# Optimization experiments

Hardware: AMD Instinct MI355X
Metric: run time of the kernel (lower is better)

The kernel has to match this reference:

```python
import jax, jax.numpy as jnp
import numpy as np

B, S, H, W = 64, 32, 40, 64
SENS, UNITS, MOTOR, NA = 1283, 48, 4, 2
UNFOLDS = 6  # ncps LTC default ode_unfolds
EPS = 1e-8


def setup_inputs() -> dict:
    key = jax.random.key(0)
    ks = iter(jax.random.split(key, 40))
    u = lambda sh, lo, hi: jax.random.uniform(next(ks), sh, jnp.float32, lo, hi)
    inp = {}
    inp["depth_image"] = jax.random.uniform(next(ks), (B, S, H, W), jnp.float32)
    inp["relative_position"] = jax.random.normal(next(ks), (B, S, 3), jnp.float32)
    # CNN params (conv k3 s2 p1 + ReLU) x3: 1->32->64->32
    def cw(o, i):
        return jax.random.normal(next(ks), (o, i, 3, 3), jnp.float32) / np.sqrt(i * 9.0)
    inp["w1"], inp["b1"] = cw(32, 1), jnp.zeros((32,), jnp.float32)
    inp["w2"], inp["b2"] = cw(64, 32), jnp.zeros((64,), jnp.float32)
    inp["w3"], inp["b3"] = cw(32, 64), jnp.zeros((32,), jnp.float32)
    # LTC cell params (ncps init ranges)
    inp["input_w"] = jnp.ones((SENS,), jnp.float32)
    inp["input_b"] = jnp.zeros((SENS,), jnp.float32)
    inp["sens_w"] = u((SENS, UNITS), 0.001, 1.0)
    inp["sens_mu"] = u((SENS, UNITS), 0.3, 0.8)
    inp["sens_sigma"] = u((SENS, UNITS), 3.0, 8.0)
    inp["sens_erev"] = jnp.sign(jax.random.normal(next(ks), (SENS, UNITS)))
    inp["rec_w"] = u((UNITS, UNITS), 0.001, 1.0)
    inp["rec_mu"] = u((UNITS, UNITS), 0.3, 0.8)
    inp["rec_sigma"] = u((UNITS, UNITS), 3.0, 8.0)
    inp["rec_erev"] = jnp.sign(jax.random.normal(next(ks), (UNITS, UNITS)))
    inp["gleak"] = u((UNITS,), 0.001, 1.0)
    inp["vleak"] = u((UNITS,), -0.2, 0.2)
    inp["cm"] = u((UNITS,), 0.4, 0.6)
    inp["out_w"] = jnp.ones((MOTOR,), jnp.float32)
    inp["out_b"] = jnp.zeros((MOTOR,), jnp.float32)
    inp["head_w"] = jax.random.normal(next(ks), (MOTOR, NA), jnp.float32) * 0.5
    inp["head_b"] = jnp.zeros((NA,), jnp.float32)
    inp["sens_mask"] = (jax.random.uniform(next(ks), (SENS, UNITS)) < 0.3).astype(jnp.int32)
    inp["rec_mask"] = (jax.random.uniform(next(ks), (UNITS, UNITS)) < 0.3).astype(jnp.int32)
    return inp


def _conv(x, w, b):
    y = jax.lax.conv_general_dilated(x, w, (2, 2), [(1, 1), (1, 1)],
                                     dimension_numbers=("NCHW", "OIHW", "NCHW"))
    return jax.nn.relu(y + b[None, :, None, None])


def reference(depth_image, relative_position, w1, b1, w2, b2, w3, b3,
              input_w, input_b, sens_w, sens_mu, sens_sigma, sens_erev,
              rec_w, rec_mu, rec_sigma, rec_erev, gleak, vleak, cm,
              out_w, out_b, head_w, head_b, sens_mask, rec_mask):
    b, s = depth_image.shape[:2]
    x = depth_image.reshape(b * s, 1, H, W)
    x = _conv(_conv(_conv(x, w1, b1), w2, b2), w3, b3)  # [b*s,32,5,8]
    feat = x.reshape(b, s, -1)  # [b,s,1280]
    seq = jnp.concatenate([feat, relative_position.reshape(b, s, -1)], axis=2)  # [b,s,1283]

    sp = jax.nn.softplus
    smask = sens_mask.astype(seq.dtype)
    rmask = rec_mask.astype(seq.dtype)
    cm_t = sp(cm) * UNFOLDS          # cm / (elapsed_time / ode_unfolds), dt=1
    gl = sp(gleak)
    sw_pos = sp(sens_w) * smask
    rw_pos = sp(rec_w) * rmask

    def step(v, xt):  # xt: [b, SENS]
        I = xt * input_w + input_b
        # sensory synapse activations: [b, SENS, UNITS]
        sa = sw_pos * jax.nn.sigmoid(sens_sigma * (I[:, :, None] - sens_mu))
        w_num_s = (sa * sens_erev).sum(1)  # [b, UNITS]
        w_den_s = sa.sum(1)
        def unfold(v, _):
            ra = rw_pos * jax.nn.sigmoid(rec_sigma * (v[:, :, None] - rec_mu))
            num = cm_t * v + gl * vleak + (ra * rec_erev).sum(1) + w_num_s
            den = cm_t + gl + ra.sum(1) + w_den_s
            return num / (den + EPS), None
        v, _ = jax.lax.scan(unfold, v, None, length=UNFOLDS)
        y = v[:, :MOTOR] * out_w + out_b  # motor neuron readout
        return v, y

    v0 = jnp.zeros((b, UNITS), seq.dtype)
    _, ys = jax.lax.scan(step, v0, jnp.swapaxes(seq, 0, 1))  # [s, b, MOTOR]
    pooled = ys.mean(0)  # mean over seq dim
    return jnp.tanh(pooled @ head_w + head_b)  # [b, NA] action mean
```

## Files before the change

kernel.cpp:

```cpp
#include <hip/hip_runtime.h>
#include <hip/hip_bf16.h>


typedef __attribute__((ext_vector_type(8))) short bshort8;
typedef __attribute__((ext_vector_type(4))) float f32x4;

constexpr long OFF_SEQ  = 0;
constexpr long OFF_SP4  = 2627584;
constexpr long OFF_RP4  = 2873920;
constexpr long OFF_CM   = 2886208;
constexpr long OFF_W2B  = 2886400;
constexpr long OFF_W3B  = 2898688;
constexpr long OFF_PART = 2907904;

__device__ __forceinline__ float sp_(float x) {
    return fmaxf(x, 0.f) + log1pf(expf(-fabsf(x)));
}

__global__ void prep_kernel(const float* __restrict__ sens_w, const float* __restrict__ sens_mu,
                            const float* __restrict__ sens_sigma, const float* __restrict__ sens_erev,
                            const int* __restrict__ sens_mask,
                            const float* __restrict__ rec_w, const float* __restrict__ rec_mu,
                            const float* __restrict__ rec_sigma, const float* __restrict__ rec_erev,
                            const int* __restrict__ rec_mask,
                            const float* __restrict__ gleak, const float* __restrict__ vleak,
                            const float* __restrict__ cm,
                            const float* __restrict__ w2, const float* __restrict__ w3,
                            float* __restrict__ ws) {
    const float L2E = 1.4426950408889634f;
    int i = blockIdx.x * 256 + threadIdx.x;
    if (i < 61584) {
        float m  = sens_mask[i] ? 1.f : 0.f;
        float sw = sp_(sens_w[i]) * m;
        float sg = sens_sigma[i], mu = sens_mu[i];
        ((float4*)(ws + OFF_SP4))[i] =
            make_float4(-sg * L2E, sg * mu * L2E, sw * sens_erev[i], sw);
    } else if (i < 64656) {
        int q = i - 61584;
        int j = q >> 6, u = q & 63;
        float4 v = make_float4(0.f, 0.f, 0.f, 0.f);
        if (u < 48) {
            int idx = j * 48 + u;
            float m  = rec_mask[idx] ? 1.f : 0.f;
            float sw = sp_(rec_w[idx]) * m;
            float sg = rec_sigma[idx], mu = rec_mu[idx];
            v = make_float4(-sg * L2E, sg * mu * L2E, sw * rec_erev[idx], sw);
        }
        ((float4*)(ws + OFF_RP4))[q] = v;
    } else if (i < 64704) {
        int u = i - 64656;
        float g = sp_(gleak[u]);
        ws[OFF_CM + u]       = sp_(cm[u]) * 6.f;
        ws[OFF_CM + 64 + u]  = g;
        ws[OFF_CM + 128 + u] = g * vleak[u];
    } else if (i < 89280) {
        int n = i - 64704;
        int j = n & 7, l = (n >> 3) & 63, t2 = n >> 9;
        int wv = t2 & 3;
        int r  = t2 >> 2;
        int xp = r & 1, hk = r >> 1;
        int ky = hk % 3, h = hk / 3;
        int oc = wv * 16 + (l & 15);
        int kgB = l >> 4;
        int icl = (kgB & 1) * 8 + j;
        int ic = h * 16 + icl;
        int kx = 2 * xp + (kgB >> 1);
        float val = (kx == 3) ? 0.f : w2[((oc * 32 + ic) * 3 + ky) * 3 + kx];
        ((__hip_bfloat16*)(ws + OFF_W2B))[n] = __float2bfloat16(val);
    } else if (i < 107712) {
        int n = i - 89280;
        int j = n & 7, l = (n >> 3) & 63, t3 = n >> 9;
        int h = t3 & 1, u2 = t3 >> 1;
        int nt = u2 / 9, p = u2 % 9;
        int ky = p / 3, kx = p % 3;
        int oc = nt * 16 + (l & 15);
        int ic = h * 32 + (l >> 4) * 8 + j;
        ((__hip_bfloat16*)(ws + OFF_W3B))[n] =
            __float2bfloat16(w3[((oc * 64 + ic) * 3 + ky) * 3 + kx]);
    }
}

#define IMGB 0
#define C1H  5424
#define A2E  0
#define A2O  12672
#define SMB  28272

__global__ __launch_bounds__(256, 4) void cnn_kernel(
    const float* __restrict__ depth, const float* __restrict__ relpos,
    const float* __restrict__ w1, const float* __restrict__ b1,
    const float* __restrict__ b2, const float* __restrict__ b3,
    const __hip_bfloat16* __restrict__ w2b, const __hip_bfloat16* __restrict__ w3b,
    float* __restrict__ seq) {
    __shared__ __align__(16) char smraw[SMB];
    const int t = threadIdx.x;
    const int img = blockIdx.x;
    const int l = t & 63;
    const int wvu = __builtin_amdgcn_readfirstlane(t >> 6);
    const int m = l & 15, kg = l >> 4;

    for (int i = t; i < 7068; i += 256) ((uint*)smraw)[i] = 0u;
    __syncthreads();
    for (int i = t; i < 1280; i += 256) {
        int pos = 2 * i;
        int h = pos >> 6, w = pos & 63;
        float2 d = *(const float2*)(depth + (long)img * 2560 + pos);
        __hip_bfloat162 pk = __float22bfloat162_rn(d);
        *(__hip_bfloat162*)(smraw + IMGB + ((h + 1) * 66 + (w + 2)) * 2) = pk;
    }
    __syncthreads();

    const __hip_bfloat16* imgp = (const __hip_bfloat16*)(smraw + IMGB);
    f32x4 acc[10];
    {
        float bias = b2[wvu * 16 + m];
#pragma unroll
        for (int mt = 0; mt < 10; ++mt) acc[mt] = (f32x4){bias, bias, bias, bias};
    }

#pragma unroll 1
    for (int h = 0; h < 2; ++h) {
        const int ocb = h * 16 + wvu * 4;
        float wv4[4][9], bv4[4];
#pragma unroll
        for (int j = 0; j < 4; ++j) {
            bv4[j] = b1[ocb + j];
#pragma unroll
            for (int k = 0; k < 9; ++k) wv4[j][k] = w1[(ocb + j) * 9 + k];
        }
#pragma unroll 1
        for (int i = 0; i < 10; ++i) {
            int p = l + (i << 6);
            int y1 = p >> 5, x1 = p & 31;
            float xin[9];
#pragma unroll
            for (int ky = 0; ky < 3; ++ky)
#pragma unroll
                for (int kx = 0; kx < 3; ++kx)
                    xin[ky * 3 + kx] = __bfloat162float(imgp[(2 * y1 + ky) * 66 + 2 * x1 + kx + 1]);
            float o[4];
#pragma unroll
            for (int j = 0; j < 4; ++j) {
                float a = bv4[j];
#pragma unroll
                for (int k = 0; k < 9; ++k) a = fmaf(wv4[j][k], xin[k], a);
                o[j] = fmaxf(a, 0.f);
            }
            char* cb = smraw + C1H + (((y1 + 1) * 34) + (x1 + 1)) * 32 + wvu * 8;
            *(__hip_bfloat162*)cb       = __float22bfloat162_rn(make_float2(o[0], o[1]));
            *(__hip_bfloat162*)(cb + 4) = __float22bfloat162_rn(make_float2(o[2], o[3]));
        }
        bshort8 Bh[6];
#pragma unroll
        for (int f = 0; f < 6; ++f)
            Bh[f] = *(const bshort8*)(w2b + (((h * 6 + f) * 4 + wvu) * 64 + l) * 8);
        __syncthreads();
#pragma unroll
        for (int ky = 0; ky < 3; ++ky) {
#pragma unroll
            for (int xp = 0; xp < 2; ++xp) {
                bshort8 Bp = Bh[ky * 2 + xp];
                const char* base = smraw + C1H + (ky * 34 + 2 * m + 2 * xp + (kg >> 1)) * 32 + (kg & 1) * 16;
#pragma unroll
                for (int mt = 0; mt < 10; ++mt) {
                    bshort8 A = *(const bshort8*)(base + mt * 2176);
                    acc[mt] = __builtin_amdgcn_mfma_f32_16x16x32_bf16(A, Bp, acc[mt], 0, 0, 0);
                }
            }
        }
        __syncthreads();
    }

    for (int i = t; i < 6336; i += 256) ((uint*)smraw)[i] = 0u;
    __syncthreads();
    {
        int oc = wvu * 16 + m;
        int q = oc >> 3, sub = oc & 7;
#pragma unroll
        for (int mt = 0; mt < 10; ++mt) {
            int row = mt + 1;
#pragma unroll
            for (int reg = 0; reg < 4; ++reg) {
                int x2 = kg * 4 + reg;
                int odd = x2 & 1;
                int xi = odd ? ((x2 + 1) >> 1) : (x2 >> 1);
                char* ab = smraw + (odd ? A2O : A2E);
                float v = fmaxf(acc[mt][reg], 0.f);
                *(__hip_bfloat16*)(ab + (((q * 11 + row) * 9 + xi) * 8 + sub) * 2) = __float2bfloat16(v);
            }
        }
    }
    __syncthreads();

    {
        const int nt = wvu & 1;
        const bool two = wvu < 2;
        f32x4 c3a = (f32x4){0.f, 0.f, 0.f, 0.f};
        f32x4 c3b = (f32x4){0.f, 0.f, 0.f, 0.f};
        const int xb = m & 7, yb = m >> 3;
#pragma unroll
        for (int p = 0; p < 9; ++p) {
            int ky = p / 3, kx = p % 3;
            const char* arr = smraw + ((kx == 1) ? A2E : A2O);
            int xi3 = xb + (kx == 2);
#pragma unroll
            for (int h = 0; h < 2; ++h) {
                bshort8 B = *(const bshort8*)(w3b + (((nt * 9 + p) * 2 + h) * 64 + l) * 8);
                int q = h * 4 + kg;
                const char* base = arr + ((q * 11 + 2 * yb + ky) * 9 + xi3) * 16;
                if (two) {
                    bshort8 A0 = *(const bshort8*)(base);
                    c3a = __builtin_amdgcn_mfma_f32_16x16x32_bf16(A0, B, c3a, 0, 0, 0);
                    bshort8 A2 = *(const bshort8*)(base + 1152);
                    c3b = __builtin_amdgcn_mfma_f32_16x16x32_bf16(A2, B, c3b, 0, 0, 0);
                } else {
                    bshort8 A1 = *(const bshort8*)(base + 576);
                    c3a = __builtin_amdgcn_mfma_f32_16x16x32_bf16(A1, B, c3a, 0, 0, 0);
                }
            }
        }
        __syncthreads();
        float* sb = (float*)smraw;
        int oc = nt * 16 + m;
        float bv = b3[oc];
        int ob40 = oc * 40;
        if (two) {
#pragma unroll
            for (int reg = 0; reg < 4; ++reg) {
                sb[ob40 + kg * 4 + reg] = fmaxf(c3a[reg] + bv, 0.f);
                int px2 = 32 + kg * 4 + reg;
                if (px2 < 40) sb[ob40 + px2] = fmaxf(c3b[reg] + bv, 0.f);
            }
        } else {
#pragma unroll
            for (int reg = 0; reg < 4; ++reg)
                sb[ob40 + 16 + kg * 4 + reg] = fmaxf(c3a[reg] + bv, 0.f);
        }
        __syncthreads();
        for (int i = t; i < 1283; i += 256)
            seq[(long)img * 1283 + i] = (i < 1280) ? sb[i] : relpos[img * 3 + (i - 1280)];
    }
}

__global__ __launch_bounds__(768) void sensory_kernel(
    const float* __restrict__ sp, const float* __restrict__ seq,
    const float* __restrict__ iw, const float* __restrict__ ibias,
    float2* __restrict__ part) {
    const float4* P4 = (const float4*)sp;
    __shared__ __align__(16) char sbuf[49152];
    float*  IT  = (float*)sbuf;
    float2* red = (float2*)sbuf;
    const int t = threadIdx.x;
    const int pb = blockIdx.x * 8;

    for (int p = 0; p < 8; ++p)
        for (int k = t; k < 1283; k += 768)
            IT[k * 8 + p] = fmaf(seq[(long)(pb + p) * 1283 + k], iw[k], ibias[k]);
    __syncthreads();

    const int u = t % 48, kg = t / 48;
    float2 acc[8];
#pragma unroll
    for (int p = 0; p < 8; ++p) acc[p] = make_float2(0.f, 0.f);

#pragma unroll 2
    for (int i = 0; i < 81; ++i) {
        int k = kg + 16 * i;
        if (k < 1283) {
            float4 pv = P4[k * 48 + u];
            float4 Ia = *(const float4*)&IT[k * 8];
            float4 Ib = *(const float4*)&IT[k * 8 + 4];
            float r0 = __builtin_amdgcn_rcpf(1.f + __builtin_amdgcn_exp2f(fmaf(pv.x, Ia.x, pv.y)));
            float r1 = __builtin_amdgcn_rcpf(1.f + __builtin_amdgcn_exp2f(fmaf(pv.x, Ia.y, pv.y)));
            float r2 = __builtin_amdgcn_rcpf(1.f + __builtin_amdgcn_exp2f(fmaf(pv.x, Ia.z, pv.y)));
            float r3 = __builtin_amdgcn_rcpf(1.f + __builtin_amdgcn_exp2f(fmaf(pv.x, Ia.w, pv.y)));
            float r4 = __builtin_amdgcn_rcpf(1.f + __builtin_amdgcn_exp2f(fmaf(pv.x, Ib.x, pv.y)));
            float r5 = __builtin_amdgcn_rcpf(1.f + __builtin_amdgcn_exp2f(fmaf(pv.x, Ib.y, pv.y)));
            float r6 = __builtin_amdgcn_rcpf(1.f + __builtin_amdgcn_exp2f(fmaf(pv.x, Ib.z, pv.y)));
            float r7 = __builtin_amdgcn_rcpf(1.f + __builtin_amdgcn_exp2f(fmaf(pv.x, Ib.w, pv.y)));
            acc[0].x = fmaf(pv.z, r0, acc[0].x); acc[0].y = fmaf(pv.w, r0, acc[0].y);
            acc[1].x = fmaf(pv.z, r1, acc[1].x); acc[1].y = fmaf(pv.w, r1, acc[1].y);
            acc[2].x = fmaf(pv.z, r2, acc[2].x); acc[2].y = fmaf(pv.w, r2, acc[2].y);
            acc[3].x = fmaf(pv.z, r3, acc[3].x); acc[3].y = fmaf(pv.w, r3, acc[3].y);
            acc[4].x = fmaf(pv.z, r4, acc[4].x); acc[4].y = fmaf(pv.w, r4, acc[4].y);
            acc[5].x = fmaf(pv.z, r5, acc[5].x); acc[5].y = fmaf(pv.w, r5, acc[5].y);
            acc[6].x = fmaf(pv.z, r6, acc[6].x); acc[6].y = fmaf(pv.w, r6, acc[6].y);
            acc[7].x = fmaf(pv.z, r7, acc[7].x); acc[7].y = fmaf(pv.w, r7, acc[7].y);
        }
    }
    __syncthreads();
#pragma unroll
    for (int p = 0; p < 8; ++p) red[(kg * 8 + p) * 48 + u] = acc[p];
    __syncthreads();
    if (t < 384) {
        int p = t / 48, uu = t - p * 48;
        float sn = 0.f, sd = 0.f;
#pragma unroll
        for (int g = 0; g < 16; ++g) {
            float2 rr = red[(g * 8 + p) * 48 + uu];
            sn += rr.x; sd += rr.y;
        }
        part[(long)(pb + p) * 48 + uu] = make_float2(sn, sd);
    }
}

__global__ __launch_bounds__(512) void recurrent_kernel(
    const float* __restrict__ rp, const float* __restrict__ cmglv,
    const float2* __restrict__ part,
    const float* __restrict__ out_w, const float* __restrict__ out_b,
    const float* __restrict__ head_w, const float* __restrict__ head_b,
    float* __restrict__ outp) {
    const float4* RP4 = (const float4*)rp;
    __shared__ float2 WL[32 * 48];
    __shared__ float2 red[2][8][64];
    __shared__ float ym[4];
    const int t = threadIdx.x, b = blockIdx.x;
    const int u = t & 63;
    const int jg = __builtin_amdgcn_readfirstlane(t >> 6);
    const int j0 = jg * 6;
    const bool uval = u < 48;
    float4 rpj[6];
#pragma unroll
    for (int jj = 0; jj < 6; ++jj) rpj[jj] = RP4[(j0 + jj) * 64 + u];
    for (int i = t; i < 1536; i += 512) WL[i] = part[(long)b * 1536 + i];
    float cmt = 0.f, gl = 0.f, glv = 0.f;
    if (uval) { cmt = cmglv[u]; gl = cmglv[64 + u]; glv = cmglv[128 + u]; }
    float ow = 0.f, ob = 0.f;
    if (jg == 0 && u < 4) { ow = out_w[u]; ob = out_b[u]; }
    __syncthreads();

    float vn = 0.f;
    float yacc = 0.f;
    int buf = 0;
    for (int s = 0; s < 32; ++s) {
        float2 wnd = uval ? WL[s * 48 + u] : make_float2(0.f, 0.f);
#pragma unroll 1
        for (int unf = 0; unf < 6; ++unf) {
            float pn = 0.f, pd = 0.f;
#pragma unroll
            for (int jj = 0; jj < 6; ++jj) {
                float vj = __shfl(vn, j0 + jj, 64);
                float r = __builtin_amdgcn_rcpf(1.f + __builtin_amdgcn_exp2f(fmaf(rpj[jj].x, vj, rpj[jj].y)));
                pn = fmaf(rpj[jj].z, r, pn);
                pd = fmaf(rpj[jj].w, r, pd);
            }
            red[buf][jg][u] = make_float2(pn, pd);
            __syncthreads();
            float sn = 0.f, sd = 0.f;
#pragma unroll
            for (int g = 0; g < 8; ++g) {
                float2 rr = red[buf][g][u];
                sn += rr.x; sd += rr.y;
            }
            float num = fmaf(cmt, vn, glv) + sn + wnd.x;
            float den = cmt + gl + sd + wnd.y;
            vn = uval ? num / (den + 1e-8f) : 0.f;
            buf ^= 1;
        }
        if (jg == 0 && u < 4) yacc = fmaf(vn, ow, yacc) + ob;
    }
    if (jg == 0 && u < 4) ym[u] = yacc;
    __syncthreads();
    if (t < 2) {
        const float inv = 1.f / 32.f;
        float o = ym[0] * inv * head_w[t] + ym[1] * inv * head_w[2 + t] +
                  ym[2] * inv * head_w[4 + t] + ym[3] * inv * head_w[6 + t] + head_b[t];
        outp[b * 2 + t] = tanhf(o);
    }
}

extern "C" void kernel_launch(void* const* d_in, const int* in_sizes, int n_in,
                              void* d_out, int out_size, void* d_ws, size_t ws_size,
                              hipStream_t stream) {
    const float* depth      = (const float*)d_in[0];
    const float* relpos     = (const float*)d_in[1];
    const float* w1         = (const float*)d_in[2];
    const float* b1         = (const float*)d_in[3];
    const float* w2         = (const float*)d_in[4];
    const float* b2         = (const float*)d_in[5];
    const float* w3         = (const float*)d_in[6];
    const float* b3         = (const float*)d_in[7];
    const float* iw         = (const float*)d_in[8];
    const float* ibias      = (const float*)d_in[9];
    const float* sens_w     = (const float*)d_in[10];
    const float* sens_mu    = (const float*)d_in[11];
    const float* sens_sigma = (const float*)d_in[12];
    const float* sens_erev  = (const float*)d_in[13];
    const float* rec_w      = (const float*)d_in[14];
    const float* rec_mu     = (const float*)d_in[15];
    const float* rec_sigma  = (const float*)d_in[16];
    const float* rec_erev   = (const float*)d_in[17];
    const float* gleak      = (const float*)d_in[18];
    const float* vleak      = (const float*)d_in[19];
    const float* cm         = (const float*)d_in[20];
    const float* out_w      = (const float*)d_in[21];
    const float* out_b      = (const float*)d_in[22];
    const float* head_w     = (const float*)d_in[23];
    const float* head_b     = (const float*)d_in[24];
    const int*   sens_mask  = (const int*)d_in[25];
    const int*   rec_mask   = (const int*)d_in[26];

    float* ws  = (float*)d_ws;
    float* out = (float*)d_out;

    prep_kernel<<<477, 256, 0, stream>>>(sens_w, sens_mu, sens_sigma, sens_erev, sens_mask,
                                         rec_w, rec_mu, rec_sigma, rec_erev, rec_mask,
                                         gleak, vleak, cm, w2, w3, ws);
    cnn_kernel<<<2048, 256, 0, stream>>>(depth, relpos, w1, b1, b2, b3,
                                         (const __hip_bfloat16*)(ws + OFF_W2B),
                                         (const __hip_bfloat16*)(ws + OFF_W3B),
                                         ws + OFF_SEQ);
    sensory_kernel<<<256, 768, 0, stream>>>(ws + OFF_SP4, ws + OFF_SEQ, iw, ibias,
                                            (float2*)(ws + OFF_PART));
    recurrent_kernel<<<64, 512, 0, stream>>>(ws + OFF_RP4, ws + OFF_CM,
                                             (const float2*)(ws + OFF_PART),
                                             out_w, out_b, head_w, head_b, out);
}
```

Measured before the change: 296.8 us.

## Compress recurrent synapses to sparse per-unit lists and run recurrence in one wave

The prep kernel now packs each postsynaptic unit's nonzero recurrent synapses (capped at 36) into compacted parameter and source-index lists. The recurrent kernel runs as a single 64-lane wave per batch that gathers presynaptic voltages by shuffle, which removes the 8-wave LDS reduction and the per-unfold block barrier. It iterates only over the masked connections, roughly 30% of the dense work. The cap of 36 would silently drop synapses for any unit with more connections, and the division is replaced by an rcp with one Newton step.

```diff
diff --git a/kernel.cpp b/kernel.cpp
--- a/kernel.cpp
+++ b/kernel.cpp
@@ -37,16 +37,30 @@
             make_float4(-sg * L2E, sg * mu * L2E, sw * sens_erev[i], sw);
     } else if (i < 64656) {
         int q = i - 61584;
-        int j = q >> 6, u = q & 63;
-        float4 v = make_float4(0.f, 0.f, 0.f, 0.f);
-        if (u < 48) {
-            int idx = j * 48 + u;
-            float m  = rec_mask[idx] ? 1.f : 0.f;
-            float sw = sp_(rec_w[idx]) * m;
-            float sg = rec_sigma[idx], mu = rec_mu[idx];
-            v = make_float4(-sg * L2E, sg * mu * L2E, sw * rec_erev[idx], sw);
-        }
-        ((float4*)(ws + OFF_RP4))[q] = v;
+        if (q < 64) {
+            float4* rpc = (float4*)(ws + OFF_RP4);
+            int* jc = (int*)(ws + OFF_RP4 + 9216);
+            int* nz = (int*)(ws + OFF_RP4 + 11520);
+            int cnt = 0;
+            if (q < 48) {
+                for (int j = 0; j < 48; ++j) {
+                    int idx = j * 48 + q;
+                    if (rec_mask[idx] && cnt < 36) {
+                        float sw = sp_(rec_w[idx]);
+                        float sg = rec_sigma[idx], mu = rec_mu[idx];
+                        rpc[cnt * 64 + q] = make_float4(-sg * L2E, sg * mu * L2E,
+                                                        sw * rec_erev[idx], sw);
+                        jc[cnt * 64 + q] = j;
+                        ++cnt;
+                    }
+                }
+                nz[q] = cnt;
+            }
+            for (int i2 = cnt; i2 < 36; ++i2) {
+                rpc[i2 * 64 + q] = make_float4(0.f, 0.f, 0.f, 0.f);
+                jc[i2 * 64 + q] = 0;
+            }
+        }
     } else if (i < 64704) {
         int u = i - 64656;
         float g = sp_(gleak[u]);
@@ -304,67 +318,80 @@
     }
 }
 
-__global__ __launch_bounds__(512) void recurrent_kernel(
+__global__ __launch_bounds__(64) void recurrent_kernel(
     const float* __restrict__ rp, const float* __restrict__ cmglv,
     const float2* __restrict__ part,
     const float* __restrict__ out_w, const float* __restrict__ out_b,
     const float* __restrict__ head_w, const float* __restrict__ head_b,
     float* __restrict__ outp) {
+    __shared__ __align__(16) float4 RPC[36 * 64];
+    __shared__ int JC[36 * 64];
+    __shared__ float2 WL[32 * 48];
+    const int t = threadIdx.x;
+    const int b = blockIdx.x;
+    const bool uval = t < 48;
+
+    int nnz = uval ? ((const int*)(rp + 11520))[t] : 0;
+    int NJ = nnz;
+#pragma unroll
+    for (int off = 32; off; off >>= 1) NJ = max(NJ, __shfl_xor(NJ, off, 64));
+
     const float4* RP4 = (const float4*)rp;
-    __shared__ float2 WL[32 * 48];
-    __shared__ float2 red[2][8][64];
-    __shared__ float ym[4];
-    const int t = threadIdx.x, b = blockIdx.x;
-    const int u = t & 63;
-    const int jg = __builtin_amdgcn_readfirstlane(t >> 6);
-    const int j0 = jg * 6;
-    const bool uval = u < 48;
-    float4 rpj[6];
-#pragma unroll
-    for (int jj = 0; jj < 6; ++jj) rpj[jj] = RP4[(j0 + jj) * 64 + u];
-    for (int i = t; i < 1536; i += 512) WL[i] = part[(long)b * 1536 + i];
+    for (int i = t; i < NJ * 64; i += 64) RPC[i] = RP4[i];
+    const int* jsrc = (const int*)(rp + 9216);
+    for (int i = t; i < NJ * 64; i += 64) JC[i] = jsrc[i];
+    for (int i = t; i < 1536; i += 64) WL[i] = part[(long)b * 1536 + i];
+
     float cmt = 0.f, gl = 0.f, glv = 0.f;
-    if (uval) { cmt = cmglv[u]; gl = cmglv[64 + u]; glv = cmglv[128 + u]; }
+    if (uval) { cmt = cmglv[t]; gl = cmglv[64 + t]; glv = cmglv[128 + t]; }
     float ow = 0.f, ob = 0.f;
-    if (jg == 0 && u < 4) { ow = out_w[u]; ob = out_b[u]; }
-    __syncthreads();
-
-    float vn = 0.f;
-    float yacc = 0.f;
-    int buf = 0;
+    if (t < 4) { ow = out_w[t]; ob = out_b[t]; }
+    __syncthreads();
+
+    float vn = 0.f, yacc = 0.f;
+#pragma unroll 1
     for (int s = 0; s < 32; ++s) {
-        float2 wnd = uval ? WL[s * 48 + u] : make_float2(0.f, 0.f);
+        float2 wnd = uval ? WL[s * 48 + t] : make_float2(0.f, 0.f);
 #pragma unroll 1
         for (int unf = 0; unf < 6; ++unf) {
-            float pn = 0.f, pd = 0.f;
-#pragma unroll
-            for (int jj = 0; jj < 6; ++jj) {
-                float vj = __shfl(vn, j0 + jj, 64);
-                float r = __builtin_amdgcn_rcpf(1.f + __builtin_amdgcn_exp2f(fmaf(rpj[jj].x, vj, rpj[jj].y)));
-                pn = fmaf(rpj[jj].z, r, pn);
-                pd = fmaf(rpj[jj].w, r, pd);
-            }
-            red[buf][jg][u] = make_float2(pn, pd);
-            __syncthreads();
-            float sn = 0.f, sd = 0.f;
-#pragma unroll
-            for (int g = 0; g < 8; ++g) {
-                float2 rr = red[buf][g][u];
-                sn += rr.x; sd += rr.y;
-            }
-            float num = fmaf(cmt, vn, glv) + sn + wnd.x;
-            float den = cmt + gl + sd + wnd.y;
-            vn = uval ? num / (den + 1e-8f) : 0.f;
-            buf ^= 1;
-        }
-        if (jg == 0 && u < 4) yacc = fmaf(vn, ow, yacc) + ob;
-    }
-    if (jg == 0 && u < 4) ym[u] = yacc;
-    __syncthreads();
+            float pn0 = 0.f, pd0 = 0.f, pn1 = 0.f, pd1 = 0.f;
+            int i = 0;
+#pragma unroll 1
+            for (; i + 1 < NJ; i += 2) {
+                float4 p0 = RPC[i * 64 + t];
+                float4 p1 = RPC[(i + 1) * 64 + t];
+                int j0 = JC[i * 64 + t];
+                int j1 = JC[(i + 1) * 64 + t];
+                float v0 = __shfl(vn, j0, 64);
+                float v1 = __shfl(vn, j1, 64);
+                float r0 = __builtin_amdgcn_rcpf(1.f + __builtin_amdgcn_exp2f(fmaf(p0.x, v0, p0.y)));
+                float r1 = __builtin_amdgcn_rcpf(1.f + __builtin_amdgcn_exp2f(fmaf(p1.x, v1, p1.y)));
+                pn0 = fmaf(p0.z, r0, pn0); pd0 = fmaf(p0.w, r0, pd0);
+                pn1 = fmaf(p1.z, r1, pn1); pd1 = fmaf(p1.w, r1, pd1);
+            }
+            if (i < NJ) {
+                float4 p0 = RPC[i * 64 + t];
+                int j0 = JC[i * 64 + t];
+                float v0 = __shfl(vn, j0, 64);
+                float r0 = __builtin_amdgcn_rcpf(1.f + __builtin_amdgcn_exp2f(fmaf(p0.x, v0, p0.y)));
+                pn0 = fmaf(p0.z, r0, pn0); pd0 = fmaf(p0.w, r0, pd0);
+            }
+            float num = fmaf(cmt, vn, glv) + (pn0 + pn1) + wnd.x;
+            float den = cmt + gl + (pd0 + pd1) + wnd.y + 1e-8f;
+            float r = __builtin_amdgcn_rcpf(den);
+            r = r * fmaf(-den, r, 2.f);
+            vn = uval ? num * r : 0.f;
+        }
+        if (t < 4) yacc = fmaf(vn, ow, yacc) + ob;
+    }
+    float y0 = __shfl(yacc, 0, 64), y1 = __shfl(yacc, 1, 64);
+    float y2 = __shfl(yacc, 2, 64), y3 = __shfl(yacc, 3, 64);
     if (t < 2) {
         const float inv = 1.f / 32.f;
-        float o = ym[0] * inv * head_w[t] + ym[1] * inv * head_w[2 + t] +
-                  ym[2] * inv * head_w[4 + t] + ym[3] * inv * head_w[6 + t] + head_b[t];
+        float o = fmaf(y0 * inv, head_w[t],
+                  fmaf(y1 * inv, head_w[2 + t],
+                  fmaf(y2 * inv, head_w[4 + t],
+                  fmaf(y3 * inv, head_w[6 + t], head_b[t]))));
         outp[b * 2 + t] = tanhf(o);
     }
 }
@@ -412,7 +439,7 @@
                                          ws + OFF_SEQ);
     sensory_kernel<<<256, 768, 0, stream>>>(ws + OFF_SP4, ws + OFF_SEQ, iw, ibias,
                                             (float2*)(ws + OFF_PART));
-    recurrent_kernel<<<64, 512, 0, stream>>>(ws + OFF_RP4, ws + OFF_CM,
-                                             (const float2*)(ws + OFF_PART),
-                                             out_w, out_b, head_w, head_b, out);
-}
+    recurrent_kernel<<<64, 64, 0, stream>>>(ws + OFF_RP4, ws + OFF_CM,
+                                            (const float2*)(ws + OFF_PART),
+                                            out_w, out_b, head_w, head_b, out);
+}
```

Result: slower. 479.3 us (+61.5%).

## Restructure recurrent LTC kernel: two batches per block, quad-lane shuffle reduction

Applied to the files above, without the earlier changes.

The recurrent kernel now processes two batch rows per 384-thread block, with each unit handled by four lanes that each cover 12 presynaptic neurons. The reduction across those lanes uses xor shuffles instead of a shared-memory partial-sum array. The state vector is broadcast through a double-buffered shared array, and the division is replaced by rcp plus one Newton step. This targets the latency-bound serial 192-step chain by cutting per-step reduction work, at the cost of fewer blocks (32) and more registers per thread.

```diff
diff --git a/kernel.cpp b/kernel.cpp
--- a/kernel.cpp
+++ b/kernel.cpp
@@ -304,68 +304,80 @@
     }
 }
 
-__global__ __launch_bounds__(512) void recurrent_kernel(
+__global__ __launch_bounds__(384) void recurrent_kernel(
     const float* __restrict__ rp, const float* __restrict__ cmglv,
     const float2* __restrict__ part,
     const float* __restrict__ out_w, const float* __restrict__ out_b,
     const float* __restrict__ head_w, const float* __restrict__ head_b,
     float* __restrict__ outp) {
+    __shared__ float2 WL[2][1536];
+    __shared__ float  LV[2][2][64];
+    __shared__ float  ym[2][4];
+    const int t  = threadIdx.x;
+    const int bb = t / 192;
+    const int g  = t % 192;
+    const int b  = blockIdx.x * 2 + bb;
+    const int u  = g >> 2;
+    const int jq = g & 3;
+
     const float4* RP4 = (const float4*)rp;
-    __shared__ float2 WL[32 * 48];
-    __shared__ float2 red[2][8][64];
-    __shared__ float ym[4];
-    const int t = threadIdx.x, b = blockIdx.x;
-    const int u = t & 63;
-    const int jg = __builtin_amdgcn_readfirstlane(t >> 6);
-    const int j0 = jg * 6;
-    const bool uval = u < 48;
-    float4 rpj[6];
-#pragma unroll
-    for (int jj = 0; jj < 6; ++jj) rpj[jj] = RP4[(j0 + jj) * 64 + u];
-    for (int i = t; i < 1536; i += 512) WL[i] = part[(long)b * 1536 + i];
-    float cmt = 0.f, gl = 0.f, glv = 0.f;
-    if (uval) { cmt = cmglv[u]; gl = cmglv[64 + u]; glv = cmglv[128 + u]; }
+    float4 P[12];
+#pragma unroll
+    for (int r = 0; r < 12; ++r) P[r] = RP4[(jq * 12 + r) * 64 + u];
+
+    for (int i = t; i < 3072; i += 384) {
+        int lb = i / 1536, li = i - lb * 1536;
+        WL[lb][li] = part[(long)(blockIdx.x * 2 + lb) * 1536 + li];
+    }
+    if (g < 64) { LV[bb][0][g] = 0.f; LV[bb][1][g] = 0.f; }
+
+    const float cmt = cmglv[u], gl = cmglv[64 + u], glv = cmglv[128 + u];
     float ow = 0.f, ob = 0.f;
-    if (jg == 0 && u < 4) { ow = out_w[u]; ob = out_b[u]; }
-    __syncthreads();
-
-    float vn = 0.f;
-    float yacc = 0.f;
+    const bool lead = (jq == 0) && (u < 4);
+    if (lead) { ow = out_w[u]; ob = out_b[u]; }
+    __syncthreads();
+
+    float vn = 0.f, yacc = 0.f;
     int buf = 0;
+#pragma unroll 1
     for (int s = 0; s < 32; ++s) {
-        float2 wnd = uval ? WL[s * 48 + u] : make_float2(0.f, 0.f);
-#pragma unroll 1
+        float2 wnd = WL[bb][s * 48 + u];
+#pragma unroll
         for (int unf = 0; unf < 6; ++unf) {
+            const float4* lv4 = (const float4*)&LV[bb][buf][jq * 12];
+            float4 V0 = lv4[0], V1 = lv4[1], V2 = lv4[2];
+            float va[12] = {V0.x, V0.y, V0.z, V0.w, V1.x, V1.y, V1.z, V1.w,
+                            V2.x, V2.y, V2.z, V2.w};
             float pn = 0.f, pd = 0.f;
 #pragma unroll
-            for (int jj = 0; jj < 6; ++jj) {
-                float vj = __shfl(vn, j0 + jj, 64);
-                float r = __builtin_amdgcn_rcpf(1.f + __builtin_amdgcn_exp2f(fmaf(rpj[jj].x, vj, rpj[jj].y)));
-                pn = fmaf(rpj[jj].z, r, pn);
-                pd = fmaf(rpj[jj].w, r, pd);
-            }
-            red[buf][jg][u] = make_float2(pn, pd);
+            for (int r = 0; r < 12; ++r) {
+                float rr = __builtin_amdgcn_rcpf(
+                    1.f + __builtin_amdgcn_exp2f(fmaf(P[r].x, va[r], P[r].y)));
+                pn = fmaf(P[r].z, rr, pn);
+                pd = fmaf(P[r].w, rr, pd);
+            }
+            pn += __shfl_xor(pn, 1, 64); pd += __shfl_xor(pd, 1, 64);
+            pn += __shfl_xor(pn, 2, 64); pd += __shfl_xor(pd, 2, 64);
+            float num = fmaf(cmt, vn, glv) + pn + wnd.x;
+            float den = cmt + gl + pd + wnd.y + 1e-8f;
+            float r0 = __builtin_amdgcn_rcpf(den);
+            r0 = r0 * fmaf(-den, r0, 2.f);
+            vn = num * r0;
+            if (jq == 0) LV[bb][buf ^ 1][u] = vn;
             __syncthreads();
-            float sn = 0.f, sd = 0.f;
-#pragma unroll
-            for (int g = 0; g < 8; ++g) {
-                float2 rr = red[buf][g][u];
-                sn += rr.x; sd += rr.y;
-            }
-            float num = fmaf(cmt, vn, glv) + sn + wnd.x;
-            float den = cmt + gl + sd + wnd.y;
-            vn = uval ? num / (den + 1e-8f) : 0.f;
             buf ^= 1;
         }
-        if (jg == 0 && u < 4) yacc = fmaf(vn, ow, yacc) + ob;
-    }
-    if (jg == 0 && u < 4) ym[u] = yacc;
-    __syncthreads();
-    if (t < 2) {
+        if (lead) yacc = fmaf(vn, ow, yacc) + ob;
+    }
+    if (lead) ym[bb][u] = yacc;
+    __syncthreads();
+    if (g < 2) {
         const float inv = 1.f / 32.f;
-        float o = ym[0] * inv * head_w[t] + ym[1] * inv * head_w[2 + t] +
-                  ym[2] * inv * head_w[4 + t] + ym[3] * inv * head_w[6 + t] + head_b[t];
-        outp[b * 2 + t] = tanhf(o);
+        float o = fmaf(ym[bb][0] * inv, head_w[g],
+                  fmaf(ym[bb][1] * inv, head_w[2 + g],
+                  fmaf(ym[bb][2] * inv, head_w[4 + g],
+                  fmaf(ym[bb][3] * inv, head_w[6 + g], head_b[g]))));
+        outp[b * 2 + g] = tanhf(o);
     }
 }
 
@@ -412,7 +424,7 @@
                                          ws + OFF_SEQ);
     sensory_kernel<<<256, 768, 0, stream>>>(ws + OFF_SP4, ws + OFF_SEQ, iw, ibias,
                                             (float2*)(ws + OFF_PART));
-    recurrent_kernel<<<64, 512, 0, stream>>>(ws + OFF_RP4, ws + OFF_CM,
+    recurrent_kernel<<<32, 384, 0, stream>>>(ws + OFF_RP4, ws + OFF_CM,
                                              (const float2*)(ws + OFF_PART),
                                              out_w, out_b, head_w, head_b, out);
 }
```

After: 318.9 us. 1.07x slower.
